# Optimization experiments

Hardware: AMD Instinct MI355X
Metric: run time of the kernel (lower is better)

## Reference

```python
import jax, jax.numpy as jnp
import numpy as np

BN_EPS = 1e-5  # torch BatchNorm1d default


def _batchnorm(x, gamma, beta):
    # x: [B, N, H]. torch BatchNorm1d on 3D input normalizes per channel (dim 1 = N)
    # over batch and last dim, using biased variance (training mode).
    mean = jnp.mean(x, axis=(0, 2), keepdims=True)
    var = jnp.var(x, axis=(0, 2), keepdims=True)
    return gamma[None, :, None] * (x - mean) / jnp.sqrt(var + BN_EPS) + beta[None, :, None]


def setup_inputs() -> dict:
    key = jax.random.key(0)
    ks = jax.random.split(key, 8)
    B, N, D, Hd = 4, 256, 128, 256
    # symmetric Bernoulli(0.05) adjacency, zero diagonal
    raw = (jax.random.uniform(ks[0], (B, N, N)) < 0.05).astype(jnp.float32)
    A = jnp.maximum(raw, jnp.swapaxes(raw, 1, 2))
    A = A * (1.0 - jnp.eye(N, dtype=jnp.float32))
    X = jax.random.normal(ks[1], (B, N, D), dtype=jnp.float32)

    def lin(k, fi, fo):
        return (jax.random.normal(k, (fi, fo), dtype=jnp.float32) / np.sqrt(fi).astype(np.float32))

    W1 = lin(ks[2], D, Hd); b1 = jnp.zeros((Hd,), jnp.float32)
    g1 = jnp.ones((N,), jnp.float32); be1 = jnp.zeros((N,), jnp.float32)
    W2 = lin(ks[3], Hd, Hd); b2 = jnp.zeros((Hd,), jnp.float32)
    g2 = jnp.ones((N,), jnp.float32); be2 = jnp.zeros((N,), jnp.float32)
    W3 = lin(ks[4], D, Hd); b3 = jnp.zeros((Hd,), jnp.float32)
    W4 = lin(ks[5], Hd, D); b4 = jnp.zeros((D,), jnp.float32)
    eps = jnp.full((1,), 0.1, dtype=jnp.float32)  # reset_parameters: 0.1/sqrt(1)
    return dict(A=A, X=X, eps=eps, W1=W1, b1=b1, g1=g1, be1=be1,
                W2=W2, b2=b2, g2=g2, be2=be2, W3=W3, b3=b3, W4=W4, b4=b4)


def reference(A, X, eps, W1, b1, g1, be1, W2, b2, g2, be2, W3, b3, W4, b4):
    B, N, D = X.shape
    I = jnp.eye(N, dtype=A.dtype)
    # standard GIN-style propagation: ((1+eps)*I + A) @ X
    X_std = ((1.0 + eps[0]) * I[None, :, :] + A) @ X

    # triangle/pair aggregation. Original: for node i, for each neighbor pair
    # (j<k) with A[j,k] != 0, add mlp2(X[j]+X[k]).
    # Vectorized: X_pw[b,i] = sum_{j<k} A[b,i,j]*A[b,i,k]*A[b,j,k]*mlp2(X[b,j]+X[b,k])
    P = X[:, :, None, :] + X[:, None, :, :]                       # [B,N,N,D] pair sums
    Fp = jax.nn.relu(jax.nn.relu(P @ W3 + b3) @ W4 + b4)          # mlp2 (dropout p=0)
    triu = jnp.triu(jnp.ones((N, N), A.dtype), k=1)               # j<k only
    G = (A * triu)[..., None] * Fp                                # [B,N,N,D]
    X_pw = jnp.einsum('bij,bik,bjkd->bid', A, A, G)

    Xn = X_std + X_pw
    # mlp1: Linear -> Dropout(0) -> ReLU -> BN -> Linear -> Dropout(0) -> ReLU -> BN
    h = _batchnorm(jax.nn.relu(Xn @ W1 + b1), g1, be1)
    h = _batchnorm(jax.nn.relu(h @ W2 + b2), g2, be2)
    return h
```

## Files before the change

kernel.cpp:

```cpp
#include <hip/hip_runtime.h>
#include <hip/hip_bf16.h>
#include <stdint.h>

#define B 4
#define N 256
#define D 128
#define H 256
#define MAXE 4096
#define SLOTCAP 256

typedef __attribute__((ext_vector_type(8))) short bf16x8;
typedef __attribute__((ext_vector_type(4))) float f32x4;

__device__ __forceinline__ ushort f2b(float f) {
  __hip_bfloat16 h = __float2bfloat16(f);
  return *reinterpret_cast<ushort*>(&h);
}
__device__ __forceinline__ float b2f(ushort u) {
  return __uint_as_float(((unsigned)u) << 16);
}

#define SWZ(off, row) ((off) ^ (((row) & 7) << 4))

__global__ __launch_bounds__(128) void k_adj_xstd(
    const float* __restrict__ A, const float* __restrict__ X,
    const float* __restrict__ eps, const float* __restrict__ W3,
    const float* __restrict__ W4,
    uint64_t* __restrict__ adjMask, unsigned* __restrict__ deg,
    uint8_t* __restrict__ nbr, unsigned* __restrict__ rowBase,
    unsigned* __restrict__ edgeCnt, unsigned* __restrict__ edges,
    ushort* __restrict__ W3T, ushort* __restrict__ W4T,
    float* __restrict__ Xn) {
  int bid = blockIdx.x, tid = threadIdx.x;
  if (bid >= B * N) {
    int idx = (bid - B * N) * 128 + tid;
    if (idx < D * H) {
      int h = idx >> 7, c = idx & 127;
      W3T[h * D + c] = f2b(W3[c * H + h]);
    } else {
      int i2 = idx - D * H;
      int d = i2 >> 8, hh = i2 & 255;
      W4T[d * H + hh] = f2b(W4[hh * D + d]);
    }
    return;
  }
  __shared__ uint8_t nbrL[64];
  __shared__ int degL;
  int row = bid;
  int b = row >> 8, j = row & 255;
  if (tid < 64) {
    int lane = tid;
    const float* Arow = A + (size_t)row * N;
    uint64_t m0 = __ballot(Arow[lane] != 0.0f);
    uint64_t m1 = __ballot(Arow[64 + lane] != 0.0f);
    uint64_t m2 = __ballot(Arow[128 + lane] != 0.0f);
    uint64_t m3 = __ballot(Arow[192 + lane] != 0.0f);
    if (lane == 0) {
      adjMask[row * 4 + 0] = m0; adjMask[row * 4 + 1] = m1;
      adjMask[row * 4 + 2] = m2; adjMask[row * 4 + 3] = m3;
    }
    int c0 = __popcll(m0), c1 = __popcll(m1), c2 = __popcll(m2), c3 = __popcll(m3);
    int total = min(c0 + c1 + c2 + c3, 64);
    if (lane == 0) { deg[row] = (unsigned)total; degL = total; }
    uint64_t lt = (1ull << lane) - 1ull;
    uint8_t* nr = nbr + (size_t)row * 64;
    if ((m0 >> lane) & 1) { int s = __popcll(m0 & lt);              if (s < 64) { nr[s] = (uint8_t)lane;       nbrL[s] = (uint8_t)lane; } }
    if ((m1 >> lane) & 1) { int s = c0 + __popcll(m1 & lt);         if (s < 64) { nr[s] = (uint8_t)(64+lane);  nbrL[s] = (uint8_t)(64+lane); } }
    if ((m2 >> lane) & 1) { int s = c0+c1 + __popcll(m2 & lt);      if (s < 64) { nr[s] = (uint8_t)(128+lane); nbrL[s] = (uint8_t)(128+lane); } }
    if ((m3 >> lane) & 1) { int s = c0+c1+c2 + __popcll(m3 & lt);   if (s < 64) { nr[s] = (uint8_t)(192+lane); nbrL[s] = (uint8_t)(192+lane); } }
    auto gtm = [&](int c) -> uint64_t {
      int lo = j - c * 64;
      if (lo < 0) return ~0ull;
      if (lo >= 63) return 0ull;
      return ~((2ull << lo) - 1ull);
    };
    uint64_t e0 = m0 & gtm(0), e1 = m1 & gtm(1), e2 = m2 & gtm(2), e3 = m3 & gtm(3);
    int t0c = __popcll(e0), t1c = __popcll(e1), t2c = __popcll(e2);
    int et = t0c + t1c + t2c + __popcll(e3);
    unsigned base = 0;
    if (lane == 0 && et) base = atomicAdd(&edgeCnt[b], (unsigned)et);
    base = (unsigned)__shfl((int)base, 0);
    if (lane == 0) rowBase[row] = base;
    unsigned* eb = edges + (size_t)b * MAXE;
    unsigned tag = ((unsigned)j << 8);
    if ((e0 >> lane) & 1) { unsigned s = base + __popcll(e0 & lt);               if (s < MAXE) eb[s] = tag | (unsigned)lane; }
    if ((e1 >> lane) & 1) { unsigned s = base + t0c + __popcll(e1 & lt);         if (s < MAXE) eb[s] = tag | (unsigned)(64+lane); }
    if ((e2 >> lane) & 1) { unsigned s = base + t0c+t1c + __popcll(e2 & lt);     if (s < MAXE) eb[s] = tag | (unsigned)(128+lane); }
    if ((e3 >> lane) & 1) { unsigned s = base + t0c+t1c+t2c + __popcll(e3 & lt); if (s < MAXE) eb[s] = tag | (unsigned)(192+lane); }
  }
  __syncthreads();
  int d = tid;
  int dg = degL;
  const float* Xb = X + ((size_t)b * N) * D;
  float a0 = (1.0f + eps[0]) * Xb[(size_t)j * D + d];
  float a1 = 0.f, a2 = 0.f, a3 = 0.f;
  int s = 0;
  for (; s + 4 <= dg; s += 4) {
    a0 += Xb[(size_t)nbrL[s]     * D + d];
    a1 += Xb[(size_t)nbrL[s + 1] * D + d];
    a2 += Xb[(size_t)nbrL[s + 2] * D + d];
    a3 += Xb[(size_t)nbrL[s + 3] * D + d];
  }
  for (; s < dg; ++s) a0 += Xb[(size_t)nbrL[s] * D + d];
  Xn[(size_t)row * D + d] = (a0 + a1) + (a2 + a3);
}

__global__ __launch_bounds__(256) void k_edge_mlp(
    const float* __restrict__ X, const unsigned* __restrict__ edges,
    const unsigned* __restrict__ edgeCnt,
    const ushort* __restrict__ W3T, const float* __restrict__ b3,
    const ushort* __restrict__ W4T, const float* __restrict__ b4,
    ushort* __restrict__ Fp) {
  __shared__ __align__(16) char smem[12288];
  __shared__ unsigned eLds[16];
  int blk = blockIdx.x;
  int b = blk >> 8, tile = blk & 255;
  unsigned cnt = min(edgeCnt[b], (unsigned)MAXE);
  int t0 = tile * 16;
  if ((unsigned)t0 >= cnt) return;
  int nE = min(16, (int)(cnt - (unsigned)t0));
  int tid = threadIdx.x;
  int w = tid >> 6, l = tid & 63, r = l & 15, g = l >> 4;
  const float* Xb = X + ((size_t)b * N) * D;

  if (tid < 16) eLds[tid] = (tid < nE) ? edges[(size_t)b * MAXE + t0 + tid] : 0u;
  __syncthreads();
  for (int idx = tid; idx < 16 * 64; idx += 256) {
    int e = idx >> 6, cp = idx & 63;
    unsigned ev = eLds[e];
    int j = (int)((ev >> 8) & 255u), k = (int)(ev & 255u);
    float2 xa = *(const float2*)(Xb + (size_t)j * D + cp * 2);
    float2 xb = *(const float2*)(Xb + (size_t)k * D + cp * 2);
    unsigned pk = (unsigned)f2b(xa.x + xb.x) | ((unsigned)f2b(xa.y + xb.y) << 16);
    *(unsigned*)(smem + e * 256 + SWZ(cp * 4, e)) = pk;
  }
  __syncthreads();
  {
    bf16x8 afr[4];
#pragma unroll
    for (int ks = 0; ks < 4; ++ks)
      afr[ks] = *(const bf16x8*)(smem + r * 256 + SWZ(ks * 64 + g * 16, r));
    f32x4 acc[4];
#pragma unroll
    for (int t4 = 0; t4 < 4; ++t4) acc[t4] = (f32x4){0.f, 0.f, 0.f, 0.f};
#pragma unroll
    for (int t4 = 0; t4 < 4; ++t4) {
      int h0 = w * 64 + t4 * 16 + r;
#pragma unroll
      for (int ks = 0; ks < 4; ++ks) {
        bf16x8 bfr = *(const bf16x8*)(W3T + (size_t)h0 * D + ks * 32 + g * 8);
        acc[t4] = __builtin_amdgcn_mfma_f32_16x16x32_bf16(afr[ks], bfr, acc[t4], 0, 0, 0);
      }
    }
#pragma unroll
    for (int t4 = 0; t4 < 4; ++t4) {
      int h0 = w * 64 + t4 * 16 + r;
      float bb = b3[h0];
#pragma unroll
      for (int jj = 0; jj < 4; ++jj) {
        int e = g * 4 + jj;
        float v = fmaxf(acc[t4][jj] + bb, 0.0f);
        *(ushort*)(smem + 4096 + e * 512 + SWZ(h0 * 2, e)) = f2b(v);
      }
    }
  }
  __syncthreads();
  {
    f32x4 acc2[2];
    acc2[0] = (f32x4){0.f, 0.f, 0.f, 0.f};
    acc2[1] = (f32x4){0.f, 0.f, 0.f, 0.f};
#pragma unroll
    for (int ks = 0; ks < 8; ++ks) {
      bf16x8 af = *(const bf16x8*)(smem + 4096 + r * 512 + SWZ(ks * 64 + g * 16, r));
#pragma unroll
      for (int t2 = 0; t2 < 2; ++t2) {
        int d0 = (w * 2 + t2) * 16 + r;
        bf16x8 bfr = *(const bf16x8*)(W4T + (size_t)d0 * H + ks * 32 + g * 8);
        acc2[t2] = __builtin_amdgcn_mfma_f32_16x16x32_bf16(af, bfr, acc2[t2], 0, 0, 0);
      }
    }
#pragma unroll
    for (int t2 = 0; t2 < 2; ++t2) {
      int d0 = (w * 2 + t2) * 16 + r;
      float bb = b4[d0];
#pragma unroll
      for (int jj = 0; jj < 4; ++jj) {
        int e = g * 4 + jj;
        if (e < nE) {
          float v = fmaxf(acc2[t2][jj] + bb, 0.0f);
          Fp[((size_t)b * MAXE + t0 + e) * D + d0] = f2b(v);
        }
      }
    }
  }
}

__global__ __launch_bounds__(256) void k_tail(
    const float* __restrict__ Xn, const ushort* __restrict__ Fp,
    const uint64_t* __restrict__ adjMask, const unsigned* __restrict__ rowBase,
    const unsigned* __restrict__ deg, const uint8_t* __restrict__ nbr,
    const float* __restrict__ W1, const float* __restrict__ b1,
    const float* __restrict__ g1, const float* __restrict__ be1,
    const float* __restrict__ W2, const float* __restrict__ b2,
    const float* __restrict__ g2, const float* __restrict__ be2,
    float* __restrict__ out) {
  __shared__ ushort slotsL[B][SLOTCAP];
  __shared__ int    listLen[B];
  __shared__ float  xr[B][D];
  __shared__ float  zr[B][H];
  __shared__ float  redS[4], redQ[4], bcast[2];
  int n = blockIdx.x, tid = threadIdx.x;
  int wv = tid >> 6, lane = tid & 63;

  {
    int row = wv * N + n;
    int dg = (int)deg[row];
    uint64_t own0 = adjMask[(size_t)row * 4 + 0];
    uint64_t own1 = adjMask[(size_t)row * 4 + 1];
    uint64_t own2 = adjMask[(size_t)row * 4 + 2];
    uint64_t own3 = adjMask[(size_t)row * 4 + 3];
    uint64_t ej[4] = {0, 0, 0, 0}, cmv[4] = {0, 0, 0, 0};
    unsigned rbj = 0;
    int cnt = 0;
    if (lane < dg) {
      int j = (int)nbr[(size_t)row * 64 + lane];
      const uint64_t* mj = adjMask + ((size_t)(wv * N + j)) * 4;
      rbj = rowBase[wv * N + j];
#pragma unroll
      for (int c = 0; c < 4; ++c) {
        int lo = j - c * 64;
        uint64_t gm = (lo < 0) ? ~0ull : (lo >= 63 ? 0ull : ~((2ull << lo) - 1ull));
        ej[c] = mj[c] & gm;
      }
      cmv[0] = ej[0] & own0; cmv[1] = ej[1] & own1;
      cmv[2] = ej[2] & own2; cmv[3] = ej[3] & own3;
      cnt = __popcll(cmv[0]) + __popcll(cmv[1]) + __popcll(cmv[2]) + __popcll(cmv[3]);
    }
    int off = cnt;
    for (int dd = 1; dd < 64; dd <<= 1) {
      int t = __shfl_up(off, dd);
      if (lane >= dd) off += t;
    }
    int excl = off - cnt;
    int total = __shfl(off, 63);
    if (lane == 63) listLen[wv] = min(total, SLOTCAP);
    if (lane < dg && cnt) {
      int idx = excl, pre = 0;
#pragma unroll
      for (int c = 0; c < 4; ++c) {
        uint64_t e = ej[c], m = cmv[c];
        while (m) {
          int lk = __builtin_ctzll(m);
          m &= m - 1;
          unsigned slot = rbj + (unsigned)(pre + __popcll(e & ((1ull << lk) - 1ull)));
          if (slot < (unsigned)MAXE && idx < SLOTCAP) slotsL[wv][idx++] = (ushort)slot;
        }
        pre += __popcll(e);
      }
    }
  }
  __syncthreads();

  {
    int p = tid >> 7, d = tid & 127;
#pragma unroll
    for (int t2 = 0; t2 < 2; ++t2) {
      int rr = p + t2 * 2;
      int len = listLen[rr];
      const ushort* FpB = Fp + (size_t)rr * MAXE * D;
      float a0 = Xn[((size_t)(rr * N + n)) * D + d];
      float a1 = 0.f, a2 = 0.f, a3 = 0.f;
      int s = 0;
      for (; s + 4 <= len; s += 4) {
        a0 += b2f(FpB[(size_t)slotsL[rr][s]     * D + d]);
        a1 += b2f(FpB[(size_t)slotsL[rr][s + 1] * D + d]);
        a2 += b2f(FpB[(size_t)slotsL[rr][s + 2] * D + d]);
        a3 += b2f(FpB[(size_t)slotsL[rr][s + 3] * D + d]);
      }
      for (; s < len; ++s) a0 += b2f(FpB[(size_t)slotsL[rr][s] * D + d]);
      xr[rr][d] = (a0 + a1) + (a2 + a3);
    }
  }
  __syncthreads();

  float v[B];
  {
    int h = tid;
    float a0 = b1[h], a1 = a0, a2 = a0, a3 = a0;
#pragma unroll 4
    for (int c = 0; c < D; c += 4) {
      float w0 = W1[(c + 0) * H + h];
      float w1 = W1[(c + 1) * H + h];
      float w2 = W1[(c + 2) * H + h];
      float w3 = W1[(c + 3) * H + h];
      float4 x0 = *(const float4*)&xr[0][c];
      float4 x1 = *(const float4*)&xr[1][c];
      float4 x2 = *(const float4*)&xr[2][c];
      float4 x3 = *(const float4*)&xr[3][c];
      a0 = fmaf(x0.x, w0, fmaf(x0.y, w1, fmaf(x0.z, w2, fmaf(x0.w, w3, a0))));
      a1 = fmaf(x1.x, w0, fmaf(x1.y, w1, fmaf(x1.z, w2, fmaf(x1.w, w3, a1))));
      a2 = fmaf(x2.x, w0, fmaf(x2.y, w1, fmaf(x2.z, w2, fmaf(x2.w, w3, a2))));
      a3 = fmaf(x3.x, w0, fmaf(x3.y, w1, fmaf(x3.z, w2, fmaf(x3.w, w3, a3))));
    }
    v[0] = fmaxf(a0, 0.f); v[1] = fmaxf(a1, 0.f);
    v[2] = fmaxf(a2, 0.f); v[3] = fmaxf(a3, 0.f);
  }
  {
    float s = v[0] + v[1] + v[2] + v[3];
    float q = v[0]*v[0] + v[1]*v[1] + v[2]*v[2] + v[3]*v[3];
    for (int o = 32; o; o >>= 1) { s += __shfl_down(s, o); q += __shfl_down(q, o); }
    if (lane == 0) { redS[wv] = s; redQ[wv] = q; }
    __syncthreads();
    if (tid == 0) {
      float S = redS[0] + redS[1] + redS[2] + redS[3];
      float Q = redQ[0] + redQ[1] + redQ[2] + redQ[3];
      float mean = S * (1.0f / 1024.0f);
      float var = Q * (1.0f / 1024.0f) - mean * mean;
      float inv = rsqrtf(var + 1e-5f);
      float aa = g1[blockIdx.x] * inv;
      bcast[0] = aa;
      bcast[1] = be1[blockIdx.x] - aa * mean;
    }
    __syncthreads();
    float aa = bcast[0], cc = bcast[1];
#pragma unroll
    for (int rr = 0; rr < B; ++rr) zr[rr][tid] = fmaf(aa, v[rr], cc);
  }
  __syncthreads();

  {
    int h = tid;
    float a0 = b2[h], a1 = a0, a2 = a0, a3 = a0;
#pragma unroll 4
    for (int c = 0; c < H; c += 4) {
      float w0 = W2[(c + 0) * H + h];
      float w1 = W2[(c + 1) * H + h];
      float w2 = W2[(c + 2) * H + h];
      float w3 = W2[(c + 3) * H + h];
      float4 z0 = *(const float4*)&zr[0][c];
      float4 z1 = *(const float4*)&zr[1][c];
      float4 z2 = *(const float4*)&zr[2][c];
      float4 z3 = *(const float4*)&zr[3][c];
      a0 = fmaf(z0.x, w0, fmaf(z0.y, w1, fmaf(z0.z, w2, fmaf(z0.w, w3, a0))));
      a1 = fmaf(z1.x, w0, fmaf(z1.y, w1, fmaf(z1.z, w2, fmaf(z1.w, w3, a1))));
      a2 = fmaf(z2.x, w0, fmaf(z2.y, w1, fmaf(z2.z, w2, fmaf(z2.w, w3, a2))));
      a3 = fmaf(z3.x, w0, fmaf(z3.y, w1, fmaf(z3.z, w2, fmaf(z3.w, w3, a3))));
    }
    v[0] = fmaxf(a0, 0.f); v[1] = fmaxf(a1, 0.f);
    v[2] = fmaxf(a2, 0.f); v[3] = fmaxf(a3, 0.f);
  }
  {
    float s = v[0] + v[1] + v[2] + v[3];
    float q = v[0]*v[0] + v[1]*v[1] + v[2]*v[2] + v[3]*v[3];
    for (int o = 32; o; o >>= 1) { s += __shfl_down(s, o); q += __shfl_down(q, o); }
    __syncthreads();
    if (lane == 0) { redS[wv] = s; redQ[wv] = q; }
    __syncthreads();
    if (tid == 0) {
      float S = redS[0] + redS[1] + redS[2] + redS[3];
      float Q = redQ[0] + redQ[1] + redQ[2] + redQ[3];
      float mean = S * (1.0f / 1024.0f);
      float var = Q * (1.0f / 1024.0f) - mean * mean;
      float inv = rsqrtf(var + 1e-5f);
      float aa = g2[blockIdx.x] * inv;
      bcast[0] = aa;
      bcast[1] = be2[blockIdx.x] - aa * mean;
    }
    __syncthreads();
    float aa = bcast[0], cc = bcast[1];
    int h = tid;
#pragma unroll
    for (int rr = 0; rr < B; ++rr)
      out[((size_t)(rr * N + blockIdx.x)) * H + h] = fmaf(aa, v[rr], cc);
  }
}

extern "C" void kernel_launch(void* const* d_in, const int* in_sizes, int n_in,
                              void* d_out, int out_size, void* d_ws, size_t ws_size,
                              hipStream_t stream) {
  const float* A   = (const float*)d_in[0];
  const float* X   = (const float*)d_in[1];
  const float* eps = (const float*)d_in[2];
  const float* W1  = (const float*)d_in[3];
  const float* b1  = (const float*)d_in[4];
  const float* g1  = (const float*)d_in[5];
  const float* be1 = (const float*)d_in[6];
  const float* W2  = (const float*)d_in[7];
  const float* b2  = (const float*)d_in[8];
  const float* g2  = (const float*)d_in[9];
  const float* be2 = (const float*)d_in[10];
  const float* W3  = (const float*)d_in[11];
  const float* b3  = (const float*)d_in[12];
  const float* W4  = (const float*)d_in[13];
  const float* b4  = (const float*)d_in[14];
  float* out = (float*)d_out;

  char* ws = (char*)d_ws;
  auto take = [&](size_t bytes) { char* r = ws; ws += (bytes + 255) & ~(size_t)255; return r; };
  unsigned* edgeCnt = (unsigned*)take(256);
  uint64_t* adjMask = (uint64_t*)take((size_t)B * N * 4 * 8);
  unsigned* rowBase = (unsigned*)take((size_t)B * N * 4);
  unsigned* edges   = (unsigned*)take((size_t)B * MAXE * 4);
  unsigned* deg     = (unsigned*)take((size_t)B * N * 4);
  uint8_t*  nbr     = (uint8_t*)take((size_t)B * N * 64);
  ushort*   W3T     = (ushort*)take((size_t)D * H * 2);
  ushort*   W4T     = (ushort*)take((size_t)D * H * 2);
  float*    Xn      = (float*)take((size_t)B * N * D * 4);
  ushort*   Fp      = (ushort*)take((size_t)B * MAXE * D * 2);

  hipMemsetAsync(edgeCnt, 0, 256, stream);

  k_adj_xstd<<<B * N + 512, 128, 0, stream>>>(
      A, X, eps, W3, W4, adjMask, deg, nbr, rowBase, edgeCnt, edges, W3T, W4T, Xn);
  k_edge_mlp<<<B * 256, 256, 0, stream>>>(
      X, edges, edgeCnt, W3T, b3, W4T, b4, Fp);
  k_tail<<<N, 256, 0, stream>>>(
      Xn, Fp, adjMask, rowBase, deg, nbr, W1, b1, g1, be1, W2, b2, g2, be2, out);
}
```

Baseline: 135.9 us.

## Move GIN neighbor aggregation into tail kernel and widen tail blocks to 512 threads

```diff
diff --git a/kernel.cpp b/kernel.cpp
--- a/kernel.cpp
+++ b/kernel.cpp
@@ -22,18 +22,16 @@
 
 #define SWZ(off, row) ((off) ^ (((row) & 7) << 4))
 
-__global__ __launch_bounds__(128) void k_adj_xstd(
-    const float* __restrict__ A, const float* __restrict__ X,
-    const float* __restrict__ eps, const float* __restrict__ W3,
+__global__ __launch_bounds__(64) void k_adj(
+    const float* __restrict__ A, const float* __restrict__ W3,
     const float* __restrict__ W4,
     uint64_t* __restrict__ adjMask, unsigned* __restrict__ deg,
     uint8_t* __restrict__ nbr, unsigned* __restrict__ rowBase,
     unsigned* __restrict__ edgeCnt, unsigned* __restrict__ edges,
-    ushort* __restrict__ W3T, ushort* __restrict__ W4T,
-    float* __restrict__ Xn) {
-  int bid = blockIdx.x, tid = threadIdx.x;
+    ushort* __restrict__ W3T, ushort* __restrict__ W4T) {
+  int bid = blockIdx.x, lane = threadIdx.x;
   if (bid >= B * N) {
-    int idx = (bid - B * N) * 128 + tid;
+    int idx = (bid - B * N) * 64 + lane;
     if (idx < D * H) {
       int h = idx >> 7, c = idx & 127;
       W3T[h * D + c] = f2b(W3[c * H + h]);
@@ -44,65 +42,45 @@
     }
     return;
   }
-  __shared__ uint8_t nbrL[64];
-  __shared__ int degL;
   int row = bid;
   int b = row >> 8, j = row & 255;
-  if (tid < 64) {
-    int lane = tid;
-    const float* Arow = A + (size_t)row * N;
-    uint64_t m0 = __ballot(Arow[lane] != 0.0f);
-    uint64_t m1 = __ballot(Arow[64 + lane] != 0.0f);
-    uint64_t m2 = __ballot(Arow[128 + lane] != 0.0f);
-    uint64_t m3 = __ballot(Arow[192 + lane] != 0.0f);
-    if (lane == 0) {
-      adjMask[row * 4 + 0] = m0; adjMask[row * 4 + 1] = m1;
-      adjMask[row * 4 + 2] = m2; adjMask[row * 4 + 3] = m3;
-    }
-    int c0 = __popcll(m0), c1 = __popcll(m1), c2 = __popcll(m2), c3 = __popcll(m3);
-    int total = min(c0 + c1 + c2 + c3, 64);
-    if (lane == 0) { deg[row] = (unsigned)total; degL = total; }
-    uint64_t lt = (1ull << lane) - 1ull;
-    uint8_t* nr = nbr + (size_t)row * 64;
-    if ((m0 >> lane) & 1) { int s = __popcll(m0 & lt);              if (s < 64) { nr[s] = (uint8_t)lane;       nbrL[s] = (uint8_t)lane; } }
-    if ((m1 >> lane) & 1) { int s = c0 + __popcll(m1 & lt);         if (s < 64) { nr[s] = (uint8_t)(64+lane);  nbrL[s] = (uint8_t)(64+lane); } }
-    if ((m2 >> lane) & 1) { int s = c0+c1 + __popcll(m2 & lt);      if (s < 64) { nr[s] = (uint8_t)(128+lane); nbrL[s] = (uint8_t)(128+lane); } }
-    if ((m3 >> lane) & 1) { int s = c0+c1+c2 + __popcll(m3 & lt);   if (s < 64) { nr[s] = (uint8_t)(192+lane); nbrL[s] = (uint8_t)(192+lane); } }
-    auto gtm = [&](int c) -> uint64_t {
-      int lo = j - c * 64;
-      if (lo < 0) return ~0ull;
-      if (lo >= 63) return 0ull;
-      return ~((2ull << lo) - 1ull);
-    };
-    uint64_t e0 = m0 & gtm(0), e1 = m1 & gtm(1), e2 = m2 & gtm(2), e3 = m3 & gtm(3);
-    int t0c = __popcll(e0), t1c = __popcll(e1), t2c = __popcll(e2);
-    int et = t0c + t1c + t2c + __popcll(e3);
-    unsigned base = 0;
-    if (lane == 0 && et) base = atomicAdd(&edgeCnt[b], (unsigned)et);
-    base = (unsigned)__shfl((int)base, 0);
-    if (lane == 0) rowBase[row] = base;
-    unsigned* eb = edges + (size_t)b * MAXE;
-    unsigned tag = ((unsigned)j << 8);
-    if ((e0 >> lane) & 1) { unsigned s = base + __popcll(e0 & lt);               if (s < MAXE) eb[s] = tag | (unsigned)lane; }
-    if ((e1 >> lane) & 1) { unsigned s = base + t0c + __popcll(e1 & lt);         if (s < MAXE) eb[s] = tag | (unsigned)(64+lane); }
-    if ((e2 >> lane) & 1) { unsigned s = base + t0c+t1c + __popcll(e2 & lt);     if (s < MAXE) eb[s] = tag | (unsigned)(128+lane); }
-    if ((e3 >> lane) & 1) { unsigned s = base + t0c+t1c+t2c + __popcll(e3 & lt); if (s < MAXE) eb[s] = tag | (unsigned)(192+lane); }
-  }
-  __syncthreads();
-  int d = tid;
-  int dg = degL;
-  const float* Xb = X + ((size_t)b * N) * D;
-  float a0 = (1.0f + eps[0]) * Xb[(size_t)j * D + d];
-  float a1 = 0.f, a2 = 0.f, a3 = 0.f;
-  int s = 0;
-  for (; s + 4 <= dg; s += 4) {
-    a0 += Xb[(size_t)nbrL[s]     * D + d];
-    a1 += Xb[(size_t)nbrL[s + 1] * D + d];
-    a2 += Xb[(size_t)nbrL[s + 2] * D + d];
-    a3 += Xb[(size_t)nbrL[s + 3] * D + d];
-  }
-  for (; s < dg; ++s) a0 += Xb[(size_t)nbrL[s] * D + d];
-  Xn[(size_t)row * D + d] = (a0 + a1) + (a2 + a3);
+  const float* Arow = A + (size_t)row * N;
+  uint64_t m0 = __ballot(Arow[lane] != 0.0f);
+  uint64_t m1 = __ballot(Arow[64 + lane] != 0.0f);
+  uint64_t m2 = __ballot(Arow[128 + lane] != 0.0f);
+  uint64_t m3 = __ballot(Arow[192 + lane] != 0.0f);
+  if (lane == 0) {
+    adjMask[row * 4 + 0] = m0; adjMask[row * 4 + 1] = m1;
+    adjMask[row * 4 + 2] = m2; adjMask[row * 4 + 3] = m3;
+  }
+  int c0 = __popcll(m0), c1 = __popcll(m1), c2 = __popcll(m2), c3 = __popcll(m3);
+  int total = min(c0 + c1 + c2 + c3, 64);
+  if (lane == 0) deg[row] = (unsigned)total;
+  uint64_t lt = (1ull << lane) - 1ull;
+  uint8_t* nr = nbr + (size_t)row * 64;
+  if ((m0 >> lane) & 1) { int s = __popcll(m0 & lt);              if (s < 64) nr[s] = (uint8_t)lane; }
+  if ((m1 >> lane) & 1) { int s = c0 + __popcll(m1 & lt);         if (s < 64) nr[s] = (uint8_t)(64+lane); }
+  if ((m2 >> lane) & 1) { int s = c0+c1 + __popcll(m2 & lt);      if (s < 64) nr[s] = (uint8_t)(128+lane); }
+  if ((m3 >> lane) & 1) { int s = c0+c1+c2 + __popcll(m3 & lt);   if (s < 64) nr[s] = (uint8_t)(192+lane); }
+  auto gtm = [&](int c) -> uint64_t {
+    int lo = j - c * 64;
+    if (lo < 0) return ~0ull;
+    if (lo >= 63) return 0ull;
+    return ~((2ull << lo) - 1ull);
+  };
+  uint64_t e0 = m0 & gtm(0), e1 = m1 & gtm(1), e2 = m2 & gtm(2), e3 = m3 & gtm(3);
+  int t0c = __popcll(e0), t1c = __popcll(e1), t2c = __popcll(e2);
+  int et = t0c + t1c + t2c + __popcll(e3);
+  unsigned base = 0;
+  if (lane == 0 && et) base = atomicAdd(&edgeCnt[b], (unsigned)et);
+  base = (unsigned)__shfl((int)base, 0);
+  if (lane == 0) rowBase[row] = base;
+  unsigned* eb = edges + (size_t)b * MAXE;
+  unsigned tag = ((unsigned)j << 8);
+  if ((e0 >> lane) & 1) { unsigned s = base + __popcll(e0 & lt);               if (s < MAXE) eb[s] = tag | (unsigned)lane; }
+  if ((e1 >> lane) & 1) { unsigned s = base + t0c + __popcll(e1 & lt);         if (s < MAXE) eb[s] = tag | (unsigned)(64+lane); }
+  if ((e2 >> lane) & 1) { unsigned s = base + t0c+t1c + __popcll(e2 & lt);     if (s < MAXE) eb[s] = tag | (unsigned)(128+lane); }
+  if ((e3 >> lane) & 1) { unsigned s = base + t0c+t1c+t2c + __popcll(e3 & lt); if (s < MAXE) eb[s] = tag | (unsigned)(192+lane); }
 }
 
 __global__ __launch_bounds__(256) void k_edge_mlp(
@@ -195,8 +173,9 @@
   }
 }
 
-__global__ __launch_bounds__(256) void k_tail(
-    const float* __restrict__ Xn, const ushort* __restrict__ Fp,
+__global__ __launch_bounds__(512) void k_tail(
+    const float* __restrict__ X, const float* __restrict__ eps,
+    const ushort* __restrict__ Fp,
     const uint64_t* __restrict__ adjMask, const unsigned* __restrict__ rowBase,
     const unsigned* __restrict__ deg, const uint8_t* __restrict__ nbr,
     const float* __restrict__ W1, const float* __restrict__ b1,
@@ -205,16 +184,18 @@
     const float* __restrict__ g2, const float* __restrict__ be2,
     float* __restrict__ out) {
   __shared__ ushort slotsL[B][SLOTCAP];
-  __shared__ int    listLen[B];
+  __shared__ uint8_t nbrL[B][64];
+  __shared__ int    listLen[B], degL[B];
   __shared__ float  xr[B][D];
   __shared__ float  zr[B][H];
-  __shared__ float  redS[4], redQ[4], bcast[2];
+  __shared__ float  redS[8], redQ[8], bcast[2];
   int n = blockIdx.x, tid = threadIdx.x;
   int wv = tid >> 6, lane = tid & 63;
 
-  {
+  if (wv < B) {
     int row = wv * N + n;
     int dg = (int)deg[row];
+    if (lane == 0) degL[wv] = dg;
     uint64_t own0 = adjMask[(size_t)row * 4 + 0];
     uint64_t own1 = adjMask[(size_t)row * 4 + 1];
     uint64_t own2 = adjMask[(size_t)row * 4 + 2];
@@ -224,6 +205,7 @@
     int cnt = 0;
     if (lane < dg) {
       int j = (int)nbr[(size_t)row * 64 + lane];
+      nbrL[wv][lane] = (uint8_t)j;
       const uint64_t* mj = adjMask + ((size_t)(wv * N + j)) * 4;
       rbj = rowBase[wv * N + j];
 #pragma unroll
@@ -263,57 +245,59 @@
 
   {
     int p = tid >> 7, d = tid & 127;
-#pragma unroll
-    for (int t2 = 0; t2 < 2; ++t2) {
-      int rr = p + t2 * 2;
-      int len = listLen[rr];
-      const ushort* FpB = Fp + (size_t)rr * MAXE * D;
-      float a0 = Xn[((size_t)(rr * N + n)) * D + d];
-      float a1 = 0.f, a2 = 0.f, a3 = 0.f;
-      int s = 0;
-      for (; s + 4 <= len; s += 4) {
-        a0 += b2f(FpB[(size_t)slotsL[rr][s]     * D + d]);
-        a1 += b2f(FpB[(size_t)slotsL[rr][s + 1] * D + d]);
-        a2 += b2f(FpB[(size_t)slotsL[rr][s + 2] * D + d]);
-        a3 += b2f(FpB[(size_t)slotsL[rr][s + 3] * D + d]);
-      }
-      for (; s < len; ++s) a0 += b2f(FpB[(size_t)slotsL[rr][s] * D + d]);
-      xr[rr][d] = (a0 + a1) + (a2 + a3);
-    }
-  }
-  __syncthreads();
-
-  float v[B];
-  {
-    int h = tid;
-    float a0 = b1[h], a1 = a0, a2 = a0, a3 = a0;
+    const float* Xb = X + ((size_t)p * N) * D;
+    int dg = degL[p];
+    float a0 = (1.0f + eps[0]) * Xb[(size_t)n * D + d];
+    float a1 = 0.f, a2 = 0.f, a3 = 0.f;
+    int s = 0;
+    for (; s + 4 <= dg; s += 4) {
+      a0 += Xb[(size_t)nbrL[p][s]     * D + d];
+      a1 += Xb[(size_t)nbrL[p][s + 1] * D + d];
+      a2 += Xb[(size_t)nbrL[p][s + 2] * D + d];
+      a3 += Xb[(size_t)nbrL[p][s + 3] * D + d];
+    }
+    for (; s < dg; ++s) a0 += Xb[(size_t)nbrL[p][s] * D + d];
+    int len = listLen[p];
+    const ushort* FpB = Fp + (size_t)p * MAXE * D;
+    s = 0;
+    for (; s + 4 <= len; s += 4) {
+      a0 += b2f(FpB[(size_t)slotsL[p][s]     * D + d]);
+      a1 += b2f(FpB[(size_t)slotsL[p][s + 1] * D + d]);
+      a2 += b2f(FpB[(size_t)slotsL[p][s + 2] * D + d]);
+      a3 += b2f(FpB[(size_t)slotsL[p][s + 3] * D + d]);
+    }
+    for (; s < len; ++s) a0 += b2f(FpB[(size_t)slotsL[p][s] * D + d]);
+    xr[p][d] = (a0 + a1) + (a2 + a3);
+  }
+  __syncthreads();
+
+  float v0, v1;
+  int half = tid >> 8, h = tid & 255;
+  int r0 = half * 2, r1 = half * 2 + 1;
+  {
+    float a0 = b1[h], a1 = a0;
 #pragma unroll 4
     for (int c = 0; c < D; c += 4) {
       float w0 = W1[(c + 0) * H + h];
       float w1 = W1[(c + 1) * H + h];
       float w2 = W1[(c + 2) * H + h];
       float w3 = W1[(c + 3) * H + h];
-      float4 x0 = *(const float4*)&xr[0][c];
-      float4 x1 = *(const float4*)&xr[1][c];
-      float4 x2 = *(const float4*)&xr[2][c];
-      float4 x3 = *(const float4*)&xr[3][c];
+      float4 x0 = *(const float4*)&xr[r0][c];
+      float4 x1 = *(const float4*)&xr[r1][c];
       a0 = fmaf(x0.x, w0, fmaf(x0.y, w1, fmaf(x0.z, w2, fmaf(x0.w, w3, a0))));
       a1 = fmaf(x1.x, w0, fmaf(x1.y, w1, fmaf(x1.z, w2, fmaf(x1.w, w3, a1))));
-      a2 = fmaf(x2.x, w0, fmaf(x2.y, w1, fmaf(x2.z, w2, fmaf(x2.w, w3, a2))));
-      a3 = fmaf(x3.x, w0, fmaf(x3.y, w1, fmaf(x3.z, w2, fmaf(x3.w, w3, a3))));
-    }
-    v[0] = fmaxf(a0, 0.f); v[1] = fmaxf(a1, 0.f);
-    v[2] = fmaxf(a2, 0.f); v[3] = fmaxf(a3, 0.f);
-  }
-  {
-    float s = v[0] + v[1] + v[2] + v[3];
-    float q = v[0]*v[0] + v[1]*v[1] + v[2]*v[2] + v[3]*v[3];
+    }
+    v0 = fmaxf(a0, 0.f); v1 = fmaxf(a1, 0.f);
+  }
+  {
+    float s = v0 + v1, q = v0 * v0 + v1 * v1;
     for (int o = 32; o; o >>= 1) { s += __shfl_down(s, o); q += __shfl_down(q, o); }
     if (lane == 0) { redS[wv] = s; redQ[wv] = q; }
     __syncthreads();
     if (tid == 0) {
-      float S = redS[0] + redS[1] + redS[2] + redS[3];
-      float Q = redQ[0] + redQ[1] + redQ[2] + redQ[3];
+      float S = 0.f, Q = 0.f;
+#pragma unroll
+      for (int i = 0; i < 8; ++i) { S += redS[i]; Q += redQ[i]; }
       float mean = S * (1.0f / 1024.0f);
       float var = Q * (1.0f / 1024.0f) - mean * mean;
       float inv = rsqrtf(var + 1e-5f);
@@ -323,42 +307,35 @@
     }
     __syncthreads();
     float aa = bcast[0], cc = bcast[1];
-#pragma unroll
-    for (int rr = 0; rr < B; ++rr) zr[rr][tid] = fmaf(aa, v[rr], cc);
-  }
-  __syncthreads();
-
-  {
-    int h = tid;
-    float a0 = b2[h], a1 = a0, a2 = a0, a3 = a0;
+    zr[r0][h] = fmaf(aa, v0, cc);
+    zr[r1][h] = fmaf(aa, v1, cc);
+  }
+  __syncthreads();
+
+  {
+    float a0 = b2[h], a1 = a0;
 #pragma unroll 4
     for (int c = 0; c < H; c += 4) {
       float w0 = W2[(c + 0) * H + h];
       float w1 = W2[(c + 1) * H + h];
       float w2 = W2[(c + 2) * H + h];
       float w3 = W2[(c + 3) * H + h];
-      float4 z0 = *(const float4*)&zr[0][c];
-      float4 z1 = *(const float4*)&zr[1][c];
-      float4 z2 = *(const float4*)&zr[2][c];
-      float4 z3 = *(const float4*)&zr[3][c];
+      float4 z0 = *(const float4*)&zr[r0][c];
+      float4 z1 = *(const float4*)&zr[r1][c];
       a0 = fmaf(z0.x, w0, fmaf(z0.y, w1, fmaf(z0.z, w2, fmaf(z0.w, w3, a0))));
       a1 = fmaf(z1.x, w0, fmaf(z1.y, w1, fmaf(z1.z, w2, fmaf(z1.w, w3, a1))));
-      a2 = fmaf(z2.x, w0, fmaf(z2.y, w1, fmaf(z2.z, w2, fmaf(z2.w, w3, a2))));
-      a3 = fmaf(z3.x, w0, fmaf(z3.y, w1, fmaf(z3.z, w2, fmaf(z3.w, w3, a3))));
-    }
-    v[0] = fmaxf(a0, 0.f); v[1] = fmaxf(a1, 0.f);
-    v[2] = fmaxf(a2, 0.f); v[3] = fmaxf(a3, 0.f);
-  }
-  {
-    float s = v[0] + v[1] + v[2] + v[3];
-    float q = v[0]*v[0] + v[1]*v[1] + v[2]*v[2] + v[3]*v[3];
+    }
+    v0 = fmaxf(a0, 0.f); v1 = fmaxf(a1, 0.f);
+  }
+  {
+    float s = v0 + v1, q = v0 * v0 + v1 * v1;
     for (int o = 32; o; o >>= 1) { s += __shfl_down(s, o); q += __shfl_down(q, o); }
-    __syncthreads();
     if (lane == 0) { redS[wv] = s; redQ[wv] = q; }
     __syncthreads();
     if (tid == 0) {
-      float S = redS[0] + redS[1] + redS[2] + redS[3];
-      float Q = redQ[0] + redQ[1] + redQ[2] + redQ[3];
+      float S = 0.f, Q = 0.f;
+#pragma unroll
+      for (int i = 0; i < 8; ++i) { S += redS[i]; Q += redQ[i]; }
       float mean = S * (1.0f / 1024.0f);
       float var = Q * (1.0f / 1024.0f) - mean * mean;
       float inv = rsqrtf(var + 1e-5f);
@@ -368,10 +345,8 @@
     }
     __syncthreads();
     float aa = bcast[0], cc = bcast[1];
-    int h = tid;
-#pragma unroll
-    for (int rr = 0; rr < B; ++rr)
-      out[((size_t)(rr * N + blockIdx.x)) * H + h] = fmaf(aa, v[rr], cc);
+    out[((size_t)(r0 * N + blockIdx.x)) * H + h] = fmaf(aa, v0, cc);
+    out[((size_t)(r1 * N + blockIdx.x)) * H + h] = fmaf(aa, v1, cc);
   }
 }
 
@@ -405,15 +380,14 @@
   uint8_t*  nbr     = (uint8_t*)take((size_t)B * N * 64);
   ushort*   W3T     = (ushort*)take((size_t)D * H * 2);
   ushort*   W4T     = (ushort*)take((size_t)D * H * 2);
-  float*    Xn      = (float*)take((size_t)B * N * D * 4);
   ushort*   Fp      = (ushort*)take((size_t)B * MAXE * D * 2);
 
   hipMemsetAsync(edgeCnt, 0, 256, stream);
 
-  k_adj_xstd<<<B * N + 512, 128, 0, stream>>>(
-      A, X, eps, W3, W4, adjMask, deg, nbr, rowBase, edgeCnt, edges, W3T, W4T, Xn);
+  k_adj<<<B * N + 1024, 64, 0, stream>>>(
+      A, W3, W4, adjMask, deg, nbr, rowBase, edgeCnt, edges, W3T, W4T);
   k_edge_mlp<<<B * 256, 256, 0, stream>>>(
       X, edges, edgeCnt, W3T, b3, W4T, b4, Fp);
-  k_tail<<<N, 256, 0, stream>>>(
-      Xn, Fp, adjMask, rowBase, deg, nbr, W1, b1, g1, be1, W2, b2, g2, be2, out);
-}
+  k_tail<<<N, 512, 0, stream>>>(
+      X, eps, Fp, adjMask, rowBase, deg, nbr, W1, b1, g1, be1, W2, b2, g2, be2, out);
+}
```

Result: slower. 146.7 us (+7.9%).
